# Kernel optimization log

Measured on AMD Instinct MI355X. Metric: run time of the kernel, lower is better.

The kernel has to match this reference:

```python
import jax, jax.numpy as jnp
import numpy as np

EMBED_DIM = 1024
NUM_HEADS = 16
HEAD_DIM = EMBED_DIM // NUM_HEADS
SCALE = HEAD_DIM ** -0.5


def setup_inputs() -> dict:
    key = jax.random.key(0)
    ks = jax.random.split(key, 12)
    B, S, D = 4, 2048, EMBED_DIM
    s = 0.02
    return {
        "query": jax.random.normal(ks[0], (B, S, D), jnp.float32),
        "key": jax.random.normal(ks[1], (B, S, D), jnp.float32),
        "value": jax.random.normal(ks[2], (B, S, D), jnp.float32),
        "Wq": jax.random.normal(ks[3], (D, D), jnp.float32) * s,
        "bq": jnp.zeros((D,), jnp.float32),
        "Wk": jax.random.normal(ks[4], (D, D), jnp.float32) * s,
        "bk": jnp.zeros((D,), jnp.float32),
        "Wv": jax.random.normal(ks[5], (D, D), jnp.float32) * s,
        "bv": jnp.zeros((D,), jnp.float32),
        "Wo": jax.random.normal(ks[6], (D, D), jnp.float32) * s,
        "bo": jnp.zeros((D,), jnp.float32),
    }


def reference(query, key, value, Wq, bq, Wk, bk, Wv, bv, Wo, bo):
    B, S, D = query.shape
    H, Hd = NUM_HEADS, HEAD_DIM

    # Linear projections (torch Linear: x @ W^T + b)
    q = query @ Wq.T + bq
    k = key @ Wk.T + bk
    v = value @ Wv.T + bv

    # [B, H, S, Hd]
    q = q.reshape(B, S, H, Hd).transpose(0, 2, 1, 3)
    k = k.reshape(B, -1, H, Hd).transpose(0, 2, 1, 3)
    v = v.reshape(B, -1, H, Hd).transpose(0, 2, 1, 3)

    # scores: [B, H, S, Skv]
    scores = jnp.einsum("bhsd,bhtd->bhst", q, k) * SCALE

    # is_causal=True: mask strictly upper triangle
    Skv = k.shape[2]
    causal = jnp.triu(jnp.ones((S, Skv), dtype=bool), k=1)
    scores = jnp.where(causal, -jnp.inf, scores)

    attn = jax.nn.softmax(scores, axis=-1)
    out = jnp.einsum("bhst,bhtd->bhsd", attn, v)  # [B, H, S, Hd]
    out = out.transpose(0, 2, 1, 3).reshape(B, S, D)
    output = out @ Wo.T + bo

    # need_weights=True, average_attn_weights=True -> mean over heads
    attn_weights = attn.mean(axis=1)  # [B, S, Skv]
    return output, attn_weights
```

## Files before the change

kernel.cpp:

```cpp
#include <hip/hip_runtime.h>
#include <hip/hip_bf16.h>
#include <cmath>
#include <type_traits>

#define BC     4
#define SEQ    2048
#define DMODEL 1024
#define NHEAD  16
#define HD     64
#define ASCALE 0.125f
#define LOG2E  1.44269504f

typedef __bf16 bf16x8 __attribute__((ext_vector_type(8)));
typedef __bf16 bf16x4 __attribute__((ext_vector_type(4)));
typedef float  f32x4  __attribute__((ext_vector_type(4)));

__device__ __forceinline__ f32x4 mfma16x16x32(bf16x8 a, bf16x8 b, f32x4 c) {
    return __builtin_amdgcn_mfma_f32_16x16x32_bf16(a, b, c, 0, 0, 0);
}

__device__ __forceinline__ float fexp2(float x) {
    return __builtin_amdgcn_exp2f(x);
}

__device__ __forceinline__ void gload_lds16(const __bf16* g, __bf16* l) {
    __builtin_amdgcn_global_load_lds(
        (const __attribute__((address_space(1))) void*)g,
        (__attribute__((address_space(3))) void*)l, 16, 0, 0);
}

__global__ __launch_bounds__(256) void cvt_w(const float* __restrict__ a,
                                             const float* __restrict__ b,
                                             const float* __restrict__ c,
                                             const float* __restrict__ d,
                                             __bf16* __restrict__ oa,
                                             __bf16* __restrict__ ob,
                                             __bf16* __restrict__ oc,
                                             __bf16* __restrict__ od) {
    const float* in; __bf16* out;
    if (blockIdx.y == 0)      { in = a; out = oa; }
    else if (blockIdx.y == 1) { in = b; out = ob; }
    else if (blockIdx.y == 2) { in = c; out = oc; }
    else                      { in = d; out = od; }
    const size_t i = ((size_t)blockIdx.x * 256 + threadIdx.x) * 8;
    float4 f0 = *(const float4*)(in + i);
    float4 f1 = *(const float4*)(in + i + 4);
    bf16x8 o;
    o[0] = (__bf16)f0.x; o[1] = (__bf16)f0.y; o[2] = (__bf16)f0.z; o[3] = (__bf16)f0.w;
    o[4] = (__bf16)f1.x; o[5] = (__bf16)f1.y; o[6] = (__bf16)f1.z; o[7] = (__bf16)f1.w;
    *(bf16x8*)(out + i) = o;
}

template <typename TA, typename TO, bool VT>
__global__ __launch_bounds__(256) void gemm_bt16(const TA* __restrict__ A,
                                                 const __bf16* __restrict__ W,
                                                 const float* __restrict__ bias,
                                                 TO* __restrict__ out,
                                                 float scale) {
    constexpr int K = DMODEL, N = DMODEL;
    __shared__ __bf16 As[128 * 64];
    __shared__ __bf16 Bs[128 * 64];
    const int tid = threadIdx.x;
    const int lane = tid & 63;
    const int wid = tid >> 6;
    const int lr = lane & 15;
    const int lg = lane >> 4;
    const int wr = (wid >> 1) * 64;
    const int wc = (wid & 1) * 64;
    const int bm = blockIdx.x * 128;
    const int bn = blockIdx.y * 128;

    f32x4 acc[4][4] = {};

    float4 a0[4], a1[4];
    if constexpr (std::is_same_v<TA, float>) {
        #pragma unroll
        for (int i = 0; i < 4; ++i) {
            const int p = tid + 256 * i;
            const int row = p >> 3, c = p & 7;
            const float* ap = A + (size_t)(bm + row) * K + c * 8;
            a0[i] = ((const float4*)ap)[0];
            a1[i] = ((const float4*)ap)[1];
        }
    }

    for (int k0 = 0; k0 < K; k0 += 64) {
        #pragma unroll
        for (int i = 0; i < 4; ++i) {
            const int p = tid + 256 * i;
            const int row = p >> 3, c = p & 7;
            const int csrc = ((c ^ (row & 7)) * 8);
            gload_lds16(W + (size_t)(bn + row) * K + k0 + csrc, &Bs[p * 8]);
        }
        if constexpr (std::is_same_v<TA, float>) {
            #pragma unroll
            for (int i = 0; i < 4; ++i) {
                const int p = tid + 256 * i;
                const int row = p >> 3, c = p & 7;
                bf16x8 v;
                v[0] = (__bf16)a0[i].x; v[1] = (__bf16)a0[i].y;
                v[2] = (__bf16)a0[i].z; v[3] = (__bf16)a0[i].w;
                v[4] = (__bf16)a1[i].x; v[5] = (__bf16)a1[i].y;
                v[6] = (__bf16)a1[i].z; v[7] = (__bf16)a1[i].w;
                *(bf16x8*)&As[row * 64 + ((c ^ (row & 7)) * 8)] = v;
            }
        } else {
            #pragma unroll
            for (int i = 0; i < 4; ++i) {
                const int p = tid + 256 * i;
                const int row = p >> 3, c = p & 7;
                const int csrc = ((c ^ (row & 7)) * 8);
                gload_lds16((const __bf16*)A + (size_t)(bm + row) * K + k0 + csrc, &As[p * 8]);
            }
        }
        __syncthreads();

        if constexpr (std::is_same_v<TA, float>) {
            if (k0 + 64 < K) {
                #pragma unroll
                for (int i = 0; i < 4; ++i) {
                    const int p = tid + 256 * i;
                    const int row = p >> 3, c = p & 7;
                    const float* ap = A + (size_t)(bm + row) * K + k0 + 64 + c * 8;
                    a0[i] = ((const float4*)ap)[0];
                    a1[i] = ((const float4*)ap)[1];
                }
            }
        }

        #pragma unroll
        for (int kk = 0; kk < 2; ++kk) {
            bf16x8 af[4], bfg[4];
            #pragma unroll
            for (int m = 0; m < 4; ++m) {
                const int row = wr + m * 16 + lr;
                af[m] = *(const bf16x8*)&As[row * 64 + ((kk * 4 + lg) ^ (row & 7)) * 8];
            }
            #pragma unroll
            for (int n = 0; n < 4; ++n) {
                const int row = wc + n * 16 + lr;
                bfg[n] = *(const bf16x8*)&Bs[row * 64 + ((kk * 4 + lg) ^ (row & 7)) * 8];
            }
            #pragma unroll
            for (int m = 0; m < 4; ++m)
                #pragma unroll
                for (int n = 0; n < 4; ++n)
                    acc[m][n] = mfma16x16x32(af[m], bfg[n], acc[m][n]);
        }
        __syncthreads();
    }

    #pragma unroll
    for (int n = 0; n < 4; ++n) {
        const int col = bn + wc + n * 16 + lr;
        const float bb = bias[col];
        #pragma unroll
        for (int m = 0; m < 4; ++m) {
            const int row0 = bm + wr + m * 16 + lg * 4;
            if constexpr (VT) {
                const int h = col >> 6, hd = col & 63;
                const int b = row0 >> 11, s = row0 & 2047;
                bf16x4 pk;
                #pragma unroll
                for (int r = 0; r < 4; ++r) pk[r] = (__bf16)((acc[m][n][r] + bb) * scale);
                *(bf16x4*)((__bf16*)out + (((size_t)b * NHEAD + h) * HD + hd) * SEQ + s) = pk;
            } else {
                #pragma unroll
                for (int r = 0; r < 4; ++r)
                    out[(size_t)(row0 + r) * N + col] = (TO)((acc[m][n][r] + bb) * scale);
            }
        }
    }
}

__global__ __launch_bounds__(512) void flash_fwd(const __bf16* __restrict__ q,
                                                 const __bf16* __restrict__ k,
                                                 const __bf16* __restrict__ vt,
                                                 __bf16* __restrict__ o,
                                                 float* __restrict__ mbuf,
                                                 float* __restrict__ lbuf) {
    __shared__ __bf16 Ks[2][64][64];
    __shared__ __bf16 Vs[2][64][64];
    __shared__ __bf16 Ps[8][16][64];
    const int tid = threadIdx.x;
    const int lane = tid & 63;
    const int wid = tid >> 6;
    const int lr = lane & 15;
    const int lg = lane >> 4;

    const int flat = blockIdx.x;
    const int xcd = flat & 7;
    const int slot = flat >> 3;
    const int group = xcd * 8 + (slot >> 4);
    const int b = group >> 4;
    const int h = group & 15;
    const int qt = 15 - (slot & 15);

    const int qr = qt * 128 + wid * 16;
    const int myq = qr + lr;
    const int dtile = qr >> 6;

    bf16x8 qf0, qf1;
    {
        const __bf16* qp = q + (size_t)(b * SEQ + myq) * DMODEL + h * HD + lg * 8;
        qf0 = ((const bf16x8*)qp)[0];
        qf1 = *(const bf16x8*)(qp + 32);
    }

    float m_run = -INFINITY;
    float l_run = 0.f;
    f32x4 oacc[4] = {};

    const int srow = tid >> 3;
    const int sc = tid & 7;
    const int swz = (sc ^ (srow & 7)) * 8;
    const int rsw = (lr & 7);
    const int nt = 2 * qt + 2;

    const __bf16* kbase = k + (size_t)(b * SEQ + srow) * DMODEL + h * HD + sc * 8;
    const __bf16* vbase = vt + ((size_t)(b * NHEAD + h) * HD + srow) * SEQ + sc * 8;

    {
        bf16x8 kr = *(const bf16x8*)kbase;
        bf16x8 vr = *(const bf16x8*)vbase;
        *(bf16x8*)&Ks[0][srow][swz] = kr;
        *(bf16x8*)&Vs[0][srow][swz] = vr;
    }
    __syncthreads();

    for (int t = 0; t < nt; ++t) {
        const int buf = t & 1;
        const bool pre = (t + 1 < nt);
        bf16x8 kr, vr;
        if (pre) {
            kr = *(const bf16x8*)(kbase + (size_t)(t + 1) * 64 * DMODEL);
            vr = *(const bf16x8*)(vbase + (t + 1) * 64);
        }

        if (t <= dtile) {
            f32x4 z[4];
            __builtin_amdgcn_s_setprio(1);
            #pragma unroll
            for (int ts = 0; ts < 4; ++ts) {
                bf16x8 kf0 = *(const bf16x8*)&Ks[buf][ts * 16 + lr][(lg ^ rsw) * 8];
                bf16x8 kf1 = *(const bf16x8*)&Ks[buf][ts * 16 + lr][((4 + lg) ^ rsw) * 8];
                f32x4 acc = {0.f, 0.f, 0.f, 0.f};
                acc = mfma16x16x32(kf0, qf0, acc);
                acc = mfma16x16x32(kf1, qf1, acc);
                z[ts] = acc;
            }
            __builtin_amdgcn_s_setprio(0);

            if (t == dtile) {
                #pragma unroll
                for (int ts = 0; ts < 4; ++ts)
                    #pragma unroll
                    for (int r = 0; r < 4; ++r)
                        if (t * 64 + ts * 16 + lg * 4 + r > myq) z[ts][r] = -INFINITY;
            }

            float a0 = fmaxf(fmaxf(z[0][0], z[0][1]), z[0][2]);
            float a1 = fmaxf(fmaxf(z[0][3], z[1][0]), z[1][1]);
            float a2 = fmaxf(fmaxf(z[1][2], z[1][3]), z[2][0]);
            float a3 = fmaxf(fmaxf(z[2][1], z[2][2]), z[2][3]);
            float a4 = fmaxf(fmaxf(z[3][0], z[3][1]), z[3][2]);
            float a5 = z[3][3];
            float b0 = fmaxf(fmaxf(a0, a1), a2);
            float b1 = fmaxf(fmaxf(a3, a4), a5);
            const float mt = fmaxf(b0, b1);

            if (!__all(mt <= m_run + 11.54f)) {
                float mr = fmaxf(mt, __shfl_xor(mt, 16));
                mr = fmaxf(mr, __shfl_xor(mr, 32));
                const float mnew = fmaxf(m_run, mr);
                const float alpha = fexp2(m_run - mnew);
                #pragma unroll
                for (int r = 0; r < 4; ++r) {
                    const float ar = __shfl(alpha, lg * 4 + r);
                    #pragma unroll
                    for (int hf = 0; hf < 4; ++hf) oacc[hf][r] *= ar;
                }
                l_run *= alpha;
                m_run = mnew;
            }

            float rsum = 0.f;
            #pragma unroll
            for (int ts = 0; ts < 4; ++ts) {
                bf16x4 pk;
                #pragma unroll
                for (int r = 0; r < 4; ++r) {
                    float pv = fexp2(z[ts][r] - m_run);
                    rsum += pv;
                    pk[r] = (__bf16)pv;
                }
                *(bf16x4*)&Ps[wid][lr][((ts * 2 + (lg >> 1)) ^ rsw) * 8 + (lg & 1) * 4] = pk;
            }
            l_run += rsum;

            bf16x8 pf0 = *(const bf16x8*)&Ps[wid][lr][(lg ^ rsw) * 8];
            bf16x8 pf1 = *(const bf16x8*)&Ps[wid][lr][((4 + lg) ^ rsw) * 8];
            __builtin_amdgcn_s_setprio(1);
            #pragma unroll
            for (int hf = 0; hf < 4; ++hf) {
                bf16x8 vf0 = *(const bf16x8*)&Vs[buf][hf * 16 + lr][(lg ^ rsw) * 8];
                bf16x8 vf1 = *(const bf16x8*)&Vs[buf][hf * 16 + lr][((4 + lg) ^ rsw) * 8];
                oacc[hf] = mfma16x16x32(pf0, vf0, oacc[hf]);
                oacc[hf] = mfma16x16x32(pf1, vf1, oacc[hf]);
            }
            __builtin_amdgcn_s_setprio(0);
        }

        if (pre) {
            *(bf16x8*)&Ks[buf ^ 1][srow][swz] = kr;
            *(bf16x8*)&Vs[buf ^ 1][srow][swz] = vr;
        }
        __syncthreads();
    }

    l_run += __shfl_xor(l_run, 16);
    l_run += __shfl_xor(l_run, 32);

    const float linv = 1.f / l_run;
    #pragma unroll
    for (int r = 0; r < 4; ++r) {
        const float li = __shfl(linv, lg * 4 + r);
        #pragma unroll
        for (int hf = 0; hf < 4; ++hf)
            o[(size_t)(b * SEQ + qr + lg * 4 + r) * DMODEL + h * HD + hf * 16 + lr] =
                (__bf16)(oacc[hf][r] * li);
    }
    if (lg == 0) {
        mbuf[((size_t)b * SEQ + myq) * NHEAD + h] = m_run;
        lbuf[((size_t)b * SEQ + myq) * NHEAD + h] = l_run;
    }
}

__global__ __launch_bounds__(256) void attn_weights(const __bf16* __restrict__ q,
                                                    const __bf16* __restrict__ k,
                                                    const float* __restrict__ mbuf,
                                                    const float* __restrict__ lbuf,
                                                    float* __restrict__ wout) {
    __shared__ __bf16 Ks[2][128][64];
    const int flat = blockIdx.x;
    const int xcd = flat & 7;
    const int slot = flat >> 3;
    const int gi = slot >> 5;
    const int st = slot & 31;
    const int b = gi & 3;
    const int t2 = (gi >> 2) ? (15 - xcd) : xcd;

    const int tid = threadIdx.x;
    const int lane = tid & 63;
    const int wid = tid >> 6;
    const int lr = lane & 15;
    const int lg = lane >> 4;
    const int myq = st * 64 + wid * 16 + lr;
    const int k0 = t2 * 128;

    float* wp = wout + (size_t)(b * SEQ + myq) * SEQ + k0 + lg * 4;

    if (2 * t2 > st) {
        const f32x4 zz = {0.f, 0.f, 0.f, 0.f};
        #pragma unroll
        for (int ts = 0; ts < 8; ++ts) *(f32x4*)(wp + ts * 16) = zz;
        return;
    }
    const bool needmask = (st <= 2 * t2 + 1);

    f32x4 rm[4], rl[4];
    {
        const float* mp = mbuf + ((size_t)b * SEQ + myq) * NHEAD;
        const float* lp = lbuf + ((size_t)b * SEQ + myq) * NHEAD;
        #pragma unroll
        for (int i = 0; i < 4; ++i) rm[i] = *(const f32x4*)(mp + i * 4);
        #pragma unroll
        for (int i = 0; i < 4; ++i) {
            f32x4 t = *(const f32x4*)(lp + i * 4);
            #pragma unroll
            for (int r = 0; r < 4; ++r) rl[i][r] = 1.f / (t[r] * (float)NHEAD);
        }
    }

    const int srow = tid >> 1;
    const int scb = (tid & 1) * 4;
    const int rsw = (lr & 7);
    const __bf16* krow = k + (size_t)(b * SEQ + k0 + srow) * DMODEL + scb * 8;
    const __bf16* qbase = q + (size_t)(b * SEQ + myq) * DMODEL + lg * 8;

    {
        bf16x8 kr[4];
        #pragma unroll
        for (int c = 0; c < 4; ++c) kr[c] = *(const bf16x8*)(krow + c * 8);
        #pragma unroll
        for (int c = 0; c < 4; ++c)
            *(bf16x8*)&Ks[0][srow][((scb + c) ^ (srow & 7)) * 8] = kr[c];
    }
    bf16x8 qna = ((const bf16x8*)qbase)[0];
    bf16x8 qnb = *(const bf16x8*)(qbase + 32);

    f32x4 wacc[8] = {};
    __syncthreads();

    #pragma unroll
    for (int h = 0; h < NHEAD; ++h) {
        const int cur = h & 1;
        bf16x8 kr[4];
        if (h + 1 < NHEAD) {
            const __bf16* kp = krow + (h + 1) * HD;
            #pragma unroll
            for (int c = 0; c < 4; ++c) kr[c] = *(const bf16x8*)(kp + c * 8);
        }
        const bf16x8 qf0 = qna, qf1 = qnb;
        if (h + 1 < NHEAD) {
            qna = *(const bf16x8*)(qbase + (h + 1) * HD);
            qnb = *(const bf16x8*)(qbase + (h + 1) * HD + 32);
        }
        const float rmh = rm[h >> 2][h & 3];
        const float rlh = rl[h >> 2][h & 3];

        #pragma unroll
        for (int ts = 0; ts < 8; ++ts) {
            bf16x8 kf0 = *(const bf16x8*)&Ks[cur][ts * 16 + lr][(lg ^ rsw) * 8];
            bf16x8 kf1 = *(const bf16x8*)&Ks[cur][ts * 16 + lr][((4 + lg) ^ rsw) * 8];
            f32x4 zz = {0.f, 0.f, 0.f, 0.f};
            zz = mfma16x16x32(kf0, qf0, zz);
            zz = mfma16x16x32(kf1, qf1, zz);
            if (needmask) {
                #pragma unroll
                for (int r = 0; r < 4; ++r) {
                    float e = 0.f;
                    if (k0 + ts * 16 + lg * 4 + r <= myq)
                        e = fexp2(zz[r] - rmh) * rlh;
                    wacc[ts][r] += e;
                }
            } else {
                #pragma unroll
                for (int r = 0; r < 4; ++r)
                    wacc[ts][r] += fexp2(zz[r] - rmh) * rlh;
            }
        }

        if (h + 1 < NHEAD) {
            #pragma unroll
            for (int c = 0; c < 4; ++c)
                *(bf16x8*)&Ks[cur ^ 1][srow][((scb + c) ^ (srow & 7)) * 8] = kr[c];
        }
        __syncthreads();
    }

    #pragma unroll
    for (int ts = 0; ts < 8; ++ts)
        *(f32x4*)(wp + ts * 16) = wacc[ts];
}

extern "C" void kernel_launch(void* const* d_in, const int* in_sizes, int n_in,
                              void* d_out, int out_size, void* d_ws, size_t ws_size,
                              hipStream_t stream) {
    const float* query = (const float*)d_in[0];
    const float* key_  = (const float*)d_in[1];
    const float* value = (const float*)d_in[2];
    const float* Wq = (const float*)d_in[3];
    const float* bq = (const float*)d_in[4];
    const float* Wk = (const float*)d_in[5];
    const float* bk = (const float*)d_in[6];
    const float* Wv = (const float*)d_in[7];
    const float* bv = (const float*)d_in[8];
    const float* Wo = (const float*)d_in[9];
    const float* bo = (const float*)d_in[10];
    float* out = (float*)d_out;

    const size_t nelem = (size_t)BC * SEQ * DMODEL;
    char* p = (char*)d_ws;
    const size_t mat = nelem * sizeof(__bf16);
    __bf16* qb  = (__bf16*)p; p += mat;
    __bf16* kb  = (__bf16*)p; p += mat;
    __bf16* vtb = (__bf16*)p; p += mat;
    __bf16* ob  = (__bf16*)p; p += mat;
    const size_t wmat = (size_t)DMODEL * DMODEL * sizeof(__bf16);
    __bf16* wqb = (__bf16*)p; p += wmat;
    __bf16* wkb = (__bf16*)p; p += wmat;
    __bf16* wvb = (__bf16*)p; p += wmat;
    __bf16* wob = (__bf16*)p; p += wmat;
    float* mb = (float*)p; p += (size_t)BC * NHEAD * SEQ * sizeof(float);
    float* lb = (float*)p; p += (size_t)BC * NHEAD * SEQ * sizeof(float);

    float* wout = out + nelem;

    cvt_w<<<dim3(DMODEL * DMODEL / 2048, 4), 256, 0, stream>>>(Wq, Wk, Wv, Wo, wqb, wkb, wvb, wob);

    const int M = BC * SEQ;
    dim3 gg(M / 128, DMODEL / 128);
    gemm_bt16<float, __bf16, false><<<gg, 256, 0, stream>>>(query, wqb, bq, qb, ASCALE * LOG2E);
    gemm_bt16<float, __bf16, false><<<gg, 256, 0, stream>>>(key_,  wkb, bk, kb, 1.f);
    gemm_bt16<float, __bf16, true ><<<gg, 256, 0, stream>>>(value, wvb, bv, vtb, 1.f);

    flash_fwd<<<dim3(1024), 512, 0, stream>>>(qb, kb, vtb, ob, mb, lb);
    gemm_bt16<__bf16, float, false><<<gg, 256, 0, stream>>>(ob, wob, bo, out, 1.f);

    attn_weights<<<dim3(2048), 256, 0, stream>>>(qb, kb, mb, lb, wout);
}
```

Measured before the change: 272.3 us.

## Batch QKV projections into one launch and double attn_weights block size

After: 272.4 us. Within noise of the previous version (+0.0%).

```diff
diff --git a/kernel.cpp b/kernel.cpp
--- a/kernel.cpp
+++ b/kernel.cpp
@@ -51,12 +51,130 @@
     *(bf16x8*)(out + i) = o;
 }
 
-template <typename TA, typename TO, bool VT>
-__global__ __launch_bounds__(256) void gemm_bt16(const TA* __restrict__ A,
-                                                 const __bf16* __restrict__ W,
-                                                 const float* __restrict__ bias,
-                                                 TO* __restrict__ out,
-                                                 float scale) {
+__global__ __launch_bounds__(256) void qkv_gemm(const float* __restrict__ Aq,
+                                                const float* __restrict__ Ak,
+                                                const float* __restrict__ Av,
+                                                const __bf16* __restrict__ Wqb,
+                                                const __bf16* __restrict__ Wkb,
+                                                const __bf16* __restrict__ Wvb,
+                                                const float* __restrict__ bq,
+                                                const float* __restrict__ bk,
+                                                const float* __restrict__ bv,
+                                                __bf16* __restrict__ oq,
+                                                __bf16* __restrict__ ok,
+                                                __bf16* __restrict__ ov) {
+    constexpr int K = DMODEL, N = DMODEL;
+    __shared__ __bf16 As[128 * 64];
+    __shared__ __bf16 Bs[128 * 64];
+    const int z = blockIdx.z;
+    const float* A; const __bf16* W; const float* bias; __bf16* out; float scale; bool vt;
+    if (z == 0)      { A = Aq; W = Wqb; bias = bq; out = oq; scale = ASCALE * LOG2E; vt = false; }
+    else if (z == 1) { A = Ak; W = Wkb; bias = bk; out = ok; scale = 1.f; vt = false; }
+    else             { A = Av; W = Wvb; bias = bv; out = ov; scale = 1.f; vt = true; }
+
+    const int tid = threadIdx.x;
+    const int lane = tid & 63;
+    const int wid = tid >> 6;
+    const int lr = lane & 15;
+    const int lg = lane >> 4;
+    const int wr = (wid >> 1) * 64;
+    const int wc = (wid & 1) * 64;
+    const int bm = blockIdx.x * 128;
+    const int bn = blockIdx.y * 128;
+
+    f32x4 acc[4][4] = {};
+
+    float4 a0[4], a1[4];
+    #pragma unroll
+    for (int i = 0; i < 4; ++i) {
+        const int p = tid + 256 * i;
+        const int row = p >> 3, c = p & 7;
+        const float* ap = A + (size_t)(bm + row) * K + c * 8;
+        a0[i] = ((const float4*)ap)[0];
+        a1[i] = ((const float4*)ap)[1];
+    }
+
+    for (int k0 = 0; k0 < K; k0 += 64) {
+        #pragma unroll
+        for (int i = 0; i < 4; ++i) {
+            const int p = tid + 256 * i;
+            const int row = p >> 3, c = p & 7;
+            const int csrc = ((c ^ (row & 7)) * 8);
+            gload_lds16(W + (size_t)(bn + row) * K + k0 + csrc, &Bs[p * 8]);
+        }
+        #pragma unroll
+        for (int i = 0; i < 4; ++i) {
+            const int p = tid + 256 * i;
+            const int row = p >> 3, c = p & 7;
+            bf16x8 v;
+            v[0] = (__bf16)a0[i].x; v[1] = (__bf16)a0[i].y;
+            v[2] = (__bf16)a0[i].z; v[3] = (__bf16)a0[i].w;
+            v[4] = (__bf16)a1[i].x; v[5] = (__bf16)a1[i].y;
+            v[6] = (__bf16)a1[i].z; v[7] = (__bf16)a1[i].w;
+            *(bf16x8*)&As[row * 64 + ((c ^ (row & 7)) * 8)] = v;
+        }
+        __syncthreads();
+
+        if (k0 + 64 < K) {
+            #pragma unroll
+            for (int i = 0; i < 4; ++i) {
+                const int p = tid + 256 * i;
+                const int row = p >> 3, c = p & 7;
+                const float* ap = A + (size_t)(bm + row) * K + k0 + 64 + c * 8;
+                a0[i] = ((const float4*)ap)[0];
+                a1[i] = ((const float4*)ap)[1];
+            }
+        }
+
+        #pragma unroll
+        for (int kk = 0; kk < 2; ++kk) {
+            bf16x8 af[4], bfg[4];
+            #pragma unroll
+            for (int m = 0; m < 4; ++m) {
+                const int row = wr + m * 16 + lr;
+                af[m] = *(const bf16x8*)&As[row * 64 + ((kk * 4 + lg) ^ (row & 7)) * 8];
+            }
+            #pragma unroll
+            for (int n = 0; n < 4; ++n) {
+                const int row = wc + n * 16 + lr;
+                bfg[n] = *(const bf16x8*)&Bs[row * 64 + ((kk * 4 + lg) ^ (row & 7)) * 8];
+            }
+            #pragma unroll
+            for (int m = 0; m < 4; ++m)
+                #pragma unroll
+                for (int n = 0; n < 4; ++n)
+                    acc[m][n] = mfma16x16x32(af[m], bfg[n], acc[m][n]);
+        }
+        __syncthreads();
+    }
+
+    #pragma unroll
+    for (int n = 0; n < 4; ++n) {
+        const int col = bn + wc + n * 16 + lr;
+        const float bb = bias[col];
+        #pragma unroll
+        for (int m = 0; m < 4; ++m) {
+            const int row0 = bm + wr + m * 16 + lg * 4;
+            if (vt) {
+                const int h = col >> 6, hd = col & 63;
+                const int b = row0 >> 11, s = row0 & 2047;
+                bf16x4 pk;
+                #pragma unroll
+                for (int r = 0; r < 4; ++r) pk[r] = (__bf16)((acc[m][n][r] + bb) * scale);
+                *(bf16x4*)(out + (((size_t)b * NHEAD + h) * HD + hd) * SEQ + s) = pk;
+            } else {
+                #pragma unroll
+                for (int r = 0; r < 4; ++r)
+                    out[(size_t)(row0 + r) * N + col] = (__bf16)((acc[m][n][r] + bb) * scale);
+            }
+        }
+    }
+}
+
+__global__ __launch_bounds__(256) void gemm_out(const __bf16* __restrict__ A,
+                                                const __bf16* __restrict__ W,
+                                                const float* __restrict__ bias,
+                                                float* __restrict__ out) {
     constexpr int K = DMODEL, N = DMODEL;
     __shared__ __bf16 As[128 * 64];
     __shared__ __bf16 Bs[128 * 64];
@@ -72,18 +190,6 @@
 
     f32x4 acc[4][4] = {};
 
-    float4 a0[4], a1[4];
-    if constexpr (std::is_same_v<TA, float>) {
-        #pragma unroll
-        for (int i = 0; i < 4; ++i) {
-            const int p = tid + 256 * i;
-            const int row = p >> 3, c = p & 7;
-            const float* ap = A + (size_t)(bm + row) * K + c * 8;
-            a0[i] = ((const float4*)ap)[0];
-            a1[i] = ((const float4*)ap)[1];
-        }
-    }
-
     for (int k0 = 0; k0 < K; k0 += 64) {
         #pragma unroll
         for (int i = 0; i < 4; ++i) {
@@ -91,42 +197,9 @@
             const int row = p >> 3, c = p & 7;
             const int csrc = ((c ^ (row & 7)) * 8);
             gload_lds16(W + (size_t)(bn + row) * K + k0 + csrc, &Bs[p * 8]);
-        }
-        if constexpr (std::is_same_v<TA, float>) {
-            #pragma unroll
-            for (int i = 0; i < 4; ++i) {
-                const int p = tid + 256 * i;
-                const int row = p >> 3, c = p & 7;
-                bf16x8 v;
-                v[0] = (__bf16)a0[i].x; v[1] = (__bf16)a0[i].y;
-                v[2] = (__bf16)a0[i].z; v[3] = (__bf16)a0[i].w;
-                v[4] = (__bf16)a1[i].x; v[5] = (__bf16)a1[i].y;
-                v[6] = (__bf16)a1[i].z; v[7] = (__bf16)a1[i].w;
-                *(bf16x8*)&As[row * 64 + ((c ^ (row & 7)) * 8)] = v;
-            }
-        } else {
-            #pragma unroll
-            for (int i = 0; i < 4; ++i) {
-                const int p = tid + 256 * i;
-                const int row = p >> 3, c = p & 7;
-                const int csrc = ((c ^ (row & 7)) * 8);
-                gload_lds16((const __bf16*)A + (size_t)(bm + row) * K + k0 + csrc, &As[p * 8]);
-            }
+            gload_lds16(A + (size_t)(bm + row) * K + k0 + csrc, &As[p * 8]);
         }
         __syncthreads();
-
-        if constexpr (std::is_same_v<TA, float>) {
-            if (k0 + 64 < K) {
-                #pragma unroll
-                for (int i = 0; i < 4; ++i) {
-                    const int p = tid + 256 * i;
-                    const int row = p >> 3, c = p & 7;
-                    const float* ap = A + (size_t)(bm + row) * K + k0 + 64 + c * 8;
-                    a0[i] = ((const float4*)ap)[0];
-                    a1[i] = ((const float4*)ap)[1];
-                }
-            }
-        }
 
         #pragma unroll
         for (int kk = 0; kk < 2; ++kk) {
@@ -157,18 +230,9 @@
         #pragma unroll
         for (int m = 0; m < 4; ++m) {
             const int row0 = bm + wr + m * 16 + lg * 4;
-            if constexpr (VT) {
-                const int h = col >> 6, hd = col & 63;
-                const int b = row0 >> 11, s = row0 & 2047;
-                bf16x4 pk;
-                #pragma unroll
-                for (int r = 0; r < 4; ++r) pk[r] = (__bf16)((acc[m][n][r] + bb) * scale);
-                *(bf16x4*)((__bf16*)out + (((size_t)b * NHEAD + h) * HD + hd) * SEQ + s) = pk;
-            } else {
-                #pragma unroll
-                for (int r = 0; r < 4; ++r)
-                    out[(size_t)(row0 + r) * N + col] = (TO)((acc[m][n][r] + bb) * scale);
-            }
+            #pragma unroll
+            for (int r = 0; r < 4; ++r)
+                out[(size_t)(row0 + r) * N + col] = acc[m][n][r] + bb;
         }
     }
 }
@@ -336,7 +400,7 @@
     }
 }
 
-__global__ __launch_bounds__(256) void attn_weights(const __bf16* __restrict__ q,
+__global__ __launch_bounds__(512) void attn_weights(const __bf16* __restrict__ q,
                                                     const __bf16* __restrict__ k,
                                                     const float* __restrict__ mbuf,
                                                     const float* __restrict__ lbuf,
@@ -345,8 +409,8 @@
     const int flat = blockIdx.x;
     const int xcd = flat & 7;
     const int slot = flat >> 3;
-    const int gi = slot >> 5;
-    const int st = slot & 31;
+    const int gi = slot >> 4;
+    const int st = slot & 15;
     const int b = gi & 3;
     const int t2 = (gi >> 2) ? (15 - xcd) : xcd;
 
@@ -355,18 +419,18 @@
     const int wid = tid >> 6;
     const int lr = lane & 15;
     const int lg = lane >> 4;
-    const int myq = st * 64 + wid * 16 + lr;
+    const int myq = st * 128 + wid * 16 + lr;
     const int k0 = t2 * 128;
 
     float* wp = wout + (size_t)(b * SEQ + myq) * SEQ + k0 + lg * 4;
 
-    if (2 * t2 > st) {
+    if (t2 > st) {
         const f32x4 zz = {0.f, 0.f, 0.f, 0.f};
         #pragma unroll
         for (int ts = 0; ts < 8; ++ts) *(f32x4*)(wp + ts * 16) = zz;
         return;
     }
-    const bool needmask = (st <= 2 * t2 + 1);
+    const bool needmask = (t2 == st);
 
     f32x4 rm[4], rl[4];
     {
@@ -382,18 +446,18 @@
         }
     }
 
-    const int srow = tid >> 1;
-    const int scb = (tid & 1) * 4;
+    const int srow = tid >> 2;
+    const int scb = (tid & 3) * 2;
     const int rsw = (lr & 7);
     const __bf16* krow = k + (size_t)(b * SEQ + k0 + srow) * DMODEL + scb * 8;
     const __bf16* qbase = q + (size_t)(b * SEQ + myq) * DMODEL + lg * 8;
 
     {
-        bf16x8 kr[4];
-        #pragma unroll
-        for (int c = 0; c < 4; ++c) kr[c] = *(const bf16x8*)(krow + c * 8);
-        #pragma unroll
-        for (int c = 0; c < 4; ++c)
+        bf16x8 kr[2];
+        #pragma unroll
+        for (int c = 0; c < 2; ++c) kr[c] = *(const bf16x8*)(krow + c * 8);
+        #pragma unroll
+        for (int c = 0; c < 2; ++c)
             *(bf16x8*)&Ks[0][srow][((scb + c) ^ (srow & 7)) * 8] = kr[c];
     }
     bf16x8 qna = ((const bf16x8*)qbase)[0];
@@ -405,11 +469,11 @@
     #pragma unroll
     for (int h = 0; h < NHEAD; ++h) {
         const int cur = h & 1;
-        bf16x8 kr[4];
+        bf16x8 kr[2];
         if (h + 1 < NHEAD) {
             const __bf16* kp = krow + (h + 1) * HD;
             #pragma unroll
-            for (int c = 0; c < 4; ++c) kr[c] = *(const bf16x8*)(kp + c * 8);
+            for (int c = 0; c < 2; ++c) kr[c] = *(const bf16x8*)(kp + c * 8);
         }
         const bf16x8 qf0 = qna, qf1 = qnb;
         if (h + 1 < NHEAD) {
@@ -443,7 +507,7 @@
 
         if (h + 1 < NHEAD) {
             #pragma unroll
-            for (int c = 0; c < 4; ++c)
+            for (int c = 0; c < 2; ++c)
                 *(bf16x8*)&Ks[cur ^ 1][srow][((scb + c) ^ (srow & 7)) * 8] = kr[c];
         }
         __syncthreads();
@@ -490,13 +554,11 @@
     cvt_w<<<dim3(DMODEL * DMODEL / 2048, 4), 256, 0, stream>>>(Wq, Wk, Wv, Wo, wqb, wkb, wvb, wob);
 
     const int M = BC * SEQ;
-    dim3 gg(M / 128, DMODEL / 128);
-    gemm_bt16<float, __bf16, false><<<gg, 256, 0, stream>>>(query, wqb, bq, qb, ASCALE * LOG2E);
-    gemm_bt16<float, __bf16, false><<<gg, 256, 0, stream>>>(key_,  wkb, bk, kb, 1.f);
-    gemm_bt16<float, __bf16, true ><<<gg, 256, 0, stream>>>(value, wvb, bv, vtb, 1.f);
+    qkv_gemm<<<dim3(M / 128, DMODEL / 128, 3), 256, 0, stream>>>(
+        query, key_, value, wqb, wkb, wvb, bq, bk, bv, qb, kb, vtb);
 
     flash_fwd<<<dim3(1024), 512, 0, stream>>>(qb, kb, vtb, ob, mb, lb);
-    gemm_bt16<__bf16, float, false><<<gg, 256, 0, stream>>>(ob, wob, bo, out, 1.f);
-
-    attn_weights<<<dim3(2048), 256, 0, stream>>>(qb, kb, mb, lb, wout);
-}
+    gemm_out<<<dim3(M / 128, DMODEL / 128), 256, 0, stream>>>(ob, wob, bo, out);
+
+    attn_weights<<<dim3(1024), 512, 0, stream>>>(qb, kb, mb, lb, wout);
+}
```
